# Optimization experiments

Measured on AMD Instinct MI355X. Metric: run time of the kernel, lower is better.

Reference implementation:

```python
import jax, jax.numpy as jnp
import numpy as np

# Physical parameter bounds in PARAM_NAMES order:
# [S1_max,S2_max,f_tens,f_rchr,f_base,r1,ku,c,alpha,psi,kappa,ki,ks,n,v,v_A,v_B,
#  Ac_max,b,lambda,chi,mu_t,T_rain,T_melt,melt_rate,lapse_rate,opg,MFMAX,MFMIN]
LOW = jnp.array([50.0,100.0,0.05,0.05,0.05,0.05,0.01,1.0,1.0,1.0,0.05,0.01,0.001,1.0,
                 0.001,0.001,0.001,0.05,0.001,5.0,2.0,0.01,-2.0,-2.0,1.0,-9.8,0.0,1.0,0.0],
                dtype=jnp.float32)
HIGH = jnp.array([5000.0,10000.0,0.95,0.95,0.95,0.95,1000.0,20.0,250.0,5.0,0.95,1000.0,
                  10000.0,10.0,0.25,0.25,0.25,0.95,3.0,10.0,5.0,5.0,4.0,4.0,10.0,0.0,1.0,10.0,10.0],
                 dtype=jnp.float32)
ROUTE_SHAPE = 2.5   # gamma routing shape (init kwarg)
KERNEL_LEN = 64     # routing kernel support (timesteps)
DT = 1.0
S1_INIT, S2_INIT = 50.0, 250.0  # state_init in the module


def _physical(raw_params):
    # low + (high-low)*sigmoid(raw), same as get_physical_params
    return LOW + (HIGH - LOW) * jax.nn.sigmoid(raw_params)


def _simulate(forcing, p):
    """Explicit-Euler 2-reservoir FUSE-style simulation. forcing: [T,3]=(prcp,pet,temp)."""
    S1_max, S2_max = p[0], p[1]
    f_tens, ku, c = p[2], p[6], p[7]
    ki, ks, n_exp = p[11], p[12], p[13]
    b, T_rain = p[18], p[22]

    def step(state, f):
        S1, S2 = state
        prcp, pet, temp = f[0], f[1], f[2]
        rain = jnp.where(temp > T_rain, prcp, 0.0)
        s1f = jnp.clip(S1 / S1_max, 0.0, 1.0)
        s2f = jnp.clip(S2 / S2_max, 0.0, 1.0)
        e1 = pet * jnp.minimum(s1f / f_tens, 1.0)          # tension-store evap
        qsx = rain * s1f ** b                               # saturation-excess runoff
        q12 = ku * s1f ** c                                 # percolation to lower store
        qif = ki * s1f                                      # interflow
        qb = ks * s2f ** n_exp                              # nonlinear baseflow
        S1n = jnp.clip(S1 + DT * (rain - qsx - e1 - q12 - qif), 0.0, S1_max)
        S2n = jnp.clip(S2 + DT * (q12 - qb), 0.0, S2_max)
        return (S1n, S2n), qsx + qif + qb

    init = (jnp.float32(S1_INIT), jnp.float32(S2_INIT))
    _, runoff = jax.lax.scan(step, init, forcing)
    return runoff  # [T]


def _route(runoff, shape, delay):
    """Causal gamma-kernel routing convolution (route_runoff)."""
    t = jnp.arange(KERNEL_LEN, dtype=jnp.float32) + 0.5
    theta = jnp.maximum(delay, 1e-3) / shape               # scale so mean = delay
    logk = (shape - 1.0) * jnp.log(t) - t / theta
    kern = jax.nn.softmax(logk)                            # normalized gamma weights
    return jnp.convolve(runoff, kern)[: runoff.shape[0]]   # causal conv


def reference(forcing, raw_params):
    phys = _physical(raw_params)
    runoff = _simulate(forcing, phys)
    # delay is used as a detached python float in the torch code -> stop_gradient
    delay = jax.lax.stop_gradient(phys[21])  # mu_t
    return _route(runoff, ROUTE_SHAPE, delay)


def setup_inputs() -> dict:
    key = jax.random.key(0)
    k1, k2, k3 = jax.random.split(key, 3)
    T = 131072
    prcp = jnp.maximum(jax.random.normal(k1, (T,)) * 5.0 + 2.0, 0.0)  # mm/day
    pet = jax.random.uniform(k2, (T,)) * 5.0                          # mm/day
    temp = jax.random.normal(k3, (T,)) * 8.0 + 5.0                    # deg C
    forcing = jnp.stack([prcp, pet, temp], axis=-1).astype(jnp.float32)
    raw_params = jnp.zeros((29,), dtype=jnp.float32)  # sigmoid(0)=0.5 -> mid-bounds
    return {"forcing": forcing, "raw_params": raw_params}
```

## Files before the change

### kernel.cpp

```cpp
#include <hip/hip_runtime.h>

#define KLEN 64
#define FCH 16
#define WARMUP 64
#define WIN_FC 64
#define S1_INIT_V 50.0f
#define S2_INIT_V 250.0f

__device__ __forceinline__ float fpow(float x, float e) {
    return exp2f(e * __log2f(x));
}
__device__ __forceinline__ float clamp01(float x) { return fminf(fmaxf(x, 0.0f), 1.0f); }
__device__ __forceinline__ float physp(const float* raw, int i, float lo, float hi) {
    return lo + (hi - lo) / (1.0f + __expf(-raw[i]));
}

struct F8 { float4 v[6]; };
__device__ __forceinline__ F8 load_f8(const float* __restrict__ forc, int t) {
    const float4* p = (const float4*)(forc + 3 * t);
    F8 r;
#pragma unroll
    for (int k = 0; k < 6; ++k) r.v[k] = p[k];
    return r;
}
__device__ __forceinline__ float f4c(const float4& v, int c) {
    return c == 0 ? v.x : c == 1 ? v.y : c == 2 ? v.z : v.w;
}
__device__ __forceinline__ float f8_get(const F8& f, int i) { return f4c(f.v[i >> 2], i & 3); }

#define S1_CORE(pr, pe, te, QACC)                                         \
    {                                                                     \
        float rain = (te) > Train ? (pr) : 0.0f;                          \
        float s1f = clamp01(S1 * invS1);                                  \
        float lg = __log2f(s1f);                                          \
        float e1 = (pe)*fminf(s1f * invft, 1.0f);                         \
        float qsx = rain * exp2f(b * lg);                                 \
        float q12 = ku * exp2f(cc * lg);                                  \
        float qif = ki * s1f;                                             \
        S1 = fminf(fmaxf(S1 + rain - qsx - e1 - q12 - qif, 0.0f), S1max); \
        QACC;                                                             \
    }

__global__ void __launch_bounds__(64) k_s1(
        const float* __restrict__ forc, const float* __restrict__ raw,
        float* __restrict__ s1s, float* __restrict__ q12f, float* __restrict__ Qw,
        int T, int nfine) {
    int lane = threadIdx.x;
    int j = blockIdx.x * WIN_FC + lane;
    bool active = j < nfine;

    const float S1max  = physp(raw, 0, 50.0f, 5000.0f);
    const float f_tens = physp(raw, 2, 0.05f, 0.95f);
    const float ku     = physp(raw, 6, 0.01f, 1000.0f);
    const float cc     = physp(raw, 7, 1.0f, 20.0f);
    const float ki     = physp(raw, 11, 0.01f, 1000.0f);
    const float b      = physp(raw, 18, 0.001f, 3.0f);
    const float Train  = physp(raw, 22, -2.0f, 4.0f);
    const float invS1 = 1.0f / S1max, invft = 1.0f / f_tens;

    float S1 = S1_INIT_V;
    float Q = 0.0f;
    if (active) {
        int t0 = j * FCH;
        int tend = min(t0 + FCH, T);
        int ts = max(t0 - WARMUP, 0);

        int ngw = (t0 - ts) >> 3;
        F8 cur = load_f8(forc, ts);
        for (int g = 0; g < ngw; ++g) {
            F8 nxt = load_f8(forc, ts + 8 * (g + 1));
#pragma unroll
            for (int s = 0; s < 8; ++s) {
                float pr = f8_get(cur, 3 * s), pe = f8_get(cur, 3 * s + 1), te = f8_get(cur, 3 * s + 2);
                S1_CORE(pr, pe, te, );
            }
            cur = nxt;
        }
        s1s[j] = S1;

        int ngm = (tend - t0) >> 3;
        for (int g = 0; g < ngm; ++g) {
            F8 nxt = load_f8(forc, t0 + 8 * min(g + 1, ngm - 1));
#pragma unroll
            for (int s = 0; s < 8; ++s) {
                float pr = f8_get(cur, 3 * s), pe = f8_get(cur, 3 * s + 1), te = f8_get(cur, 3 * s + 2);
                S1_CORE(pr, pe, te, Q += q12);
            }
            cur = nxt;
        }
        for (int t = t0 + 8 * ngm; t < tend; ++t) {
            float pr = forc[3 * t], pe = forc[3 * t + 1], te = forc[3 * t + 2];
            S1_CORE(pr, pe, te, Q += q12);
        }
        q12f[j] = Q;
    }
    float s = Q;
#pragma unroll
    for (int o = 32; o >= 1; o >>= 1) s += __shfl_xor(s, o, 64);
    if (lane == 0) Qw[blockIdx.x] = s;
}

__global__ void __launch_bounds__(64) k_s2win(
        const float* __restrict__ raw, const float* __restrict__ Qw,
        const float* __restrict__ q12f,
        float* __restrict__ S2win, float* __restrict__ qbwin,
        float* __restrict__ s2fine, int* __restrict__ flag,
        int T, int nfine) {
    int lane = threadIdx.x;
    const float S2max = physp(raw, 1, 100.0f, 10000.0f);
    const float ks    = physp(raw, 12, 0.001f, 10000.0f);
    const float nn    = physp(raw, 13, 1.0f, 10.0f);
    const float invS2 = 1.0f / S2max;

    int NW = (nfine + WIN_FC - 1) / WIN_FC;
    int WSTEPS = WIN_FC * FCH;

    int w0 = 2 * lane, w1 = 2 * lane + 1;
    float L0 = (w0 < NW) ? (float)min(WSTEPS, T - WSTEPS * w0) : 0.0f;
    float L1 = (w1 < NW) ? (float)min(WSTEPS, T - WSTEPS * w1) : 0.0f;
    float Q0 = (w0 < NW) ? Qw[w0] : 0.0f;
    float Q1 = (w1 < NW) ? Qw[w1] : 0.0f;

    float qb0 = ks * fpow(clamp01(S2_INIT_V * invS2), nn);
    float qb1 = qb0;
    float S20 = S2_INIT_V, S21 = S2_INIT_V;
    bool picard_ok = (NW <= 128);
    if (picard_ok) {
        for (int it = 0; it < 12; ++it) {
            float d0 = Q0 - L0 * qb0;
            float d1 = Q1 - L1 * qb1;
            float pair = d0 + d1;
            float sc = pair;
#pragma unroll
            for (int o = 1; o < 64; o <<= 1) {
                float v = __shfl_up(sc, o, 64);
                if (lane >= o) sc += v;
            }
            float excl = sc - pair;
            S20 = S2_INIT_V + excl;
            S21 = S20 + d0;
            qb0 = ks * fpow(clamp01(S20 * invS2), nn);
            qb1 = ks * fpow(clamp01(S21 * invS2), nn);
        }
        bool bad = false;
        if (w0 < NW) bad |= (S20 - L0 * qb0 < 0.5f) || (S20 + Q0 > S2max - 0.5f);
        if (w1 < NW) bad |= (S21 - L1 * qb1 < 0.5f) || (S21 + Q1 > S2max - 0.5f);
        picard_ok = (__ballot(bad) == 0ULL);
    }
    if (picard_ok) {
        if (w0 < NW) { S2win[w0] = S20; qbwin[w0] = qb0; }
        if (w1 < NW) { S2win[w1] = S21; qbwin[w1] = qb1; }
        if (lane == 0) *flag = 0;
    } else if (lane == 0) {
        *flag = 1;
        float S2 = S2_INIT_V;
        for (int w = 0; w < NW; ++w) {
            float s2f = clamp01(S2 * invS2);
            float qb = ks * fpow(s2f, nn);
            S2win[w] = S2; qbwin[w] = qb;
            int i0 = w * WIN_FC, i1 = min(i0 + WIN_FC, nfine);
            for (int i = i0; i < i1; ++i) {
                s2fine[i] = S2;
                float steps = (float)min(FCH, T - FCH * i);
                S2 = fminf(fmaxf(S2 + q12f[i] - steps * qb, 0.0f), S2max);
            }
        }
    }
}

__global__ void __launch_bounds__(64) k_sim(
        const float* __restrict__ forc, const float* __restrict__ raw,
        const float* __restrict__ s1s, const float* __restrict__ q12f,
        const float* __restrict__ S2win, const float* __restrict__ qbwin,
        const float* __restrict__ s2fine, const int* __restrict__ flag,
        float* __restrict__ runoff, int T, int nfine) {
    int lane = threadIdx.x;
    int j = blockIdx.x * WIN_FC + lane;
    bool active = j < nfine;

    const float S1max  = physp(raw, 0, 50.0f, 5000.0f);
    const float S2max  = physp(raw, 1, 100.0f, 10000.0f);
    const float f_tens = physp(raw, 2, 0.05f, 0.95f);
    const float ku     = physp(raw, 6, 0.01f, 1000.0f);
    const float ki     = physp(raw, 11, 0.01f, 1000.0f);
    const float ks     = physp(raw, 12, 0.001f, 10000.0f);
    const float nn     = physp(raw, 13, 1.0f, 10.0f);
    const float cc     = physp(raw, 7, 1.0f, 20.0f);
    const float b      = physp(raw, 18, 0.001f, 3.0f);
    const float Train  = physp(raw, 22, -2.0f, 4.0f);
    const float invS1 = 1.0f / S1max, invS2 = 1.0f / S2max, invft = 1.0f / f_tens;

    float q = active ? q12f[j] : 0.0f;
    float S2;
    if (*flag) {
        S2 = active ? s2fine[j] : 0.0f;
    } else {
        float sc = q;
#pragma unroll
        for (int o = 1; o < 64; o <<= 1) {
            float v = __shfl_up(sc, o, 64);
            if (lane >= o) sc += v;
        }
        float excl = sc - q;
        S2 = S2win[blockIdx.x] + excl - qbwin[blockIdx.x] * (float)(FCH * lane);
        S2 = fminf(fmaxf(S2, 0.0f), S2max);
    }
    if (!active) return;

    float S1 = s1s[j];
    int t0 = j * FCH;
    int tend = min(t0 + FCH, T);

#define SIM_CORE(pr, pe, te, EMIT)                                        \
    {                                                                     \
        float rain = (te) > Train ? (pr) : 0.0f;                          \
        float s1f = clamp01(S1 * invS1);                                  \
        float s2f = clamp01(S2 * invS2);                                  \
        float lg = __log2f(s1f);                                          \
        float e1 = (pe)*fminf(s1f * invft, 1.0f);                         \
        float qsx = rain * exp2f(b * lg);                                 \
        float q12 = ku * exp2f(cc * lg);                                  \
        float qif = ki * s1f;                                             \
        float qb = ks * fpow(s2f, nn);                                    \
        EMIT;                                                             \
        S1 = fminf(fmaxf(S1 + rain - qsx - e1 - q12 - qif, 0.0f), S1max); \
        S2 = fminf(fmaxf(S2 + q12 - qb, 0.0f), S2max);                    \
    }

    int ngm = (tend - t0) >> 3;
    if (ngm > 0) {
        F8 cur = load_f8(forc, t0);
        for (int g = 0; g < ngm; ++g) {
            F8 nxt = load_f8(forc, t0 + 8 * min(g + 1, ngm - 1));
            float ro[8];
#pragma unroll
            for (int s = 0; s < 8; ++s) {
                float pr = f8_get(cur, 3 * s), pe = f8_get(cur, 3 * s + 1), te = f8_get(cur, 3 * s + 2);
                SIM_CORE(pr, pe, te, ro[s] = qsx + qif + qb);
            }
            float4* rp = (float4*)(runoff + t0 + 8 * g);
            rp[0] = make_float4(ro[0], ro[1], ro[2], ro[3]);
            rp[1] = make_float4(ro[4], ro[5], ro[6], ro[7]);
            cur = nxt;
        }
    }
    for (int t = t0 + 8 * ngm; t < tend; ++t) {
        float pr = forc[3 * t], pe = forc[3 * t + 1], te = forc[3 * t + 2];
        SIM_CORE(pr, pe, te, runoff[t] = qsx + qif + qb);
    }
}

__global__ void k_route(const float* __restrict__ runoff, const float* __restrict__ raw,
                        float* __restrict__ out, int T) {
    __shared__ float ls[256 + KLEN - 1];
    __shared__ float ker[KLEN];
    int tid = threadIdx.x;
    int base = blockIdx.x * 256;
    if (tid < 64) {
        float delay = physp(raw, 21, 0.01f, 5.0f);
        float theta = fmaxf(delay, 1e-3f) * (1.0f / 2.5f);
        float tt = (float)tid + 0.5f;
        float logk = 1.5f * __logf(tt) - tt / theta;
        float m = logk;
#pragma unroll
        for (int o = 32; o >= 1; o >>= 1) m = fmaxf(m, __shfl_xor(m, o, 64));
        float e = __expf(logk - m);
        float s = e;
#pragma unroll
        for (int o = 32; o >= 1; o >>= 1) s += __shfl_xor(s, o, 64);
        ker[tid] = e / s;
    }
    for (int i = tid; i < 256 + KLEN - 1; i += 256) {
        int t = base - (KLEN - 1) + i;
        ls[i] = (t >= 0 && t < T) ? runoff[t] : 0.0f;
    }
    __syncthreads();
    float acc = 0.0f;
#pragma unroll
    for (int k = 0; k < KLEN; ++k) acc += ker[k] * ls[tid + (KLEN - 1) - k];
    int t = base + tid;
    if (t < T) out[t] = acc;
}

extern "C" void kernel_launch(void* const* d_in, const int* in_sizes, int n_in,
                              void* d_out, int out_size, void* d_ws, size_t ws_size,
                              hipStream_t stream) {
    const float* forcing = (const float*)d_in[0];
    const float* raw = (const float*)d_in[1];
    float* out = (float*)d_out;
    float* ws = (float*)d_ws;

    int T = in_sizes[0] / 3;
    int nfine = (T + FCH - 1) / FCH;
    int NW = (nfine + WIN_FC - 1) / WIN_FC;
    int P = ((nfine + 7) / 8) * 8;
    int PW = ((NW + 7) / 8) * 8;

    float* s1s = ws;
    float* q12f = s1s + P;
    float* Qw = q12f + P;
    float* S2win = Qw + PW;
    float* qbwin = S2win + PW;
    float* s2fine = qbwin + PW;
    int* flag = (int*)(s2fine + P);
    float* runoff = (float*)(flag + 8);

    k_s1<<<NW, 64, 0, stream>>>(forcing, raw, s1s, q12f, Qw, T, nfine);
    k_s2win<<<1, 64, 0, stream>>>(raw, Qw, q12f, S2win, qbwin, s2fine, flag, T, nfine);
    k_sim<<<NW, 64, 0, stream>>>(forcing, raw, s1s, q12f, S2win, qbwin, s2fine, flag,
                                 runoff, T, nfine);
    k_route<<<(T + 255) / 256, 256, 0, stream>>>(runoff, raw, out, T);
}
```

Before: 73.59 us.

## Fuse S1 scan, S2 window solve, simulation and routing into one cooperative kernel

Replaces the four launches (S1 chunk pass, single-block S2 Picard solve, full simulation, routing) with one cooperative kernel that uses grid.sync between phases. Each thread keeps per-step q12 and qsx+qif in registers from the S1 pass, so the second pass only recomputes the S2 recurrence instead of re-reading forcing and recomputing S1. Every block redundantly runs the small S2 window solve into shared memory, and routing runs as a grid-stride loop after a second grid sync. The cost is two grid-wide barriers, higher register pressure from the per-thread arrays, and a fallback path where each block runs a long serial loop.

```diff
diff --git a/kernel.cpp b/kernel.cpp
--- a/kernel.cpp
+++ b/kernel.cpp
@@ -1,9 +1,14 @@
 #include <hip/hip_runtime.h>
+#include <hip/hip_cooperative_groups.h>
+
+namespace cg = cooperative_groups;
 
 #define KLEN 64
 #define FCH 16
 #define WARMUP 64
 #define WIN_FC 64
+#define BLOCK 256
+#define WPB (BLOCK / 64)
 #define S1_INIT_V 50.0f
 #define S2_INIT_V 250.0f
 
@@ -41,31 +46,48 @@
         QACC;                                                             \
     }
 
-__global__ void __launch_bounds__(64) k_s1(
+__global__ void __launch_bounds__(BLOCK) k_fused(
         const float* __restrict__ forc, const float* __restrict__ raw,
-        float* __restrict__ s1s, float* __restrict__ q12f, float* __restrict__ Qw,
+        float* __restrict__ out,
+        float* __restrict__ q12f, float* __restrict__ Qw, float* __restrict__ runoff,
         int T, int nfine) {
-    int lane = threadIdx.x;
-    int j = blockIdx.x * WIN_FC + lane;
-    bool active = j < nfine;
+    cg::grid_group grid = cg::this_grid();
+
+    __shared__ float S2w_l[128], qbw_l[128];
+    __shared__ float s2f_l[BLOCK];
+    __shared__ float ker[KLEN];
+    __shared__ float ls[BLOCK + KLEN - 1];
+    __shared__ int flag_l;
+
+    const int tid = threadIdx.x;
+    const int lane = tid & 63;
+    const int wv = tid >> 6;
+    const int w = blockIdx.x * WPB + wv;
+    const int j = w * WIN_FC + lane;
+    const int NW = (nfine + WIN_FC - 1) / WIN_FC;
+    const bool active = j < nfine;
 
     const float S1max  = physp(raw, 0, 50.0f, 5000.0f);
+    const float S2max  = physp(raw, 1, 100.0f, 10000.0f);
     const float f_tens = physp(raw, 2, 0.05f, 0.95f);
     const float ku     = physp(raw, 6, 0.01f, 1000.0f);
     const float cc     = physp(raw, 7, 1.0f, 20.0f);
     const float ki     = physp(raw, 11, 0.01f, 1000.0f);
+    const float ks     = physp(raw, 12, 0.001f, 10000.0f);
+    const float nn     = physp(raw, 13, 1.0f, 10.0f);
     const float b      = physp(raw, 18, 0.001f, 3.0f);
     const float Train  = physp(raw, 22, -2.0f, 4.0f);
-    const float invS1 = 1.0f / S1max, invft = 1.0f / f_tens;
-
-    float S1 = S1_INIT_V;
+    const float invS1 = 1.0f / S1max, invS2 = 1.0f / S2max, invft = 1.0f / f_tens;
+
+    float q12s[FCH], qxi[FCH];
     float Q = 0.0f;
     if (active) {
-        int t0 = j * FCH;
-        int tend = min(t0 + FCH, T);
+        const int t0 = j * FCH;
+        const bool full = (t0 + FCH <= T);
+        float S1 = S1_INIT_V;
         int ts = max(t0 - WARMUP, 0);
-
         int ngw = (t0 - ts) >> 3;
+
         F8 cur = load_f8(forc, ts);
         for (int g = 0; g < ngw; ++g) {
             F8 nxt = load_f8(forc, ts + 8 * (g + 1));
@@ -76,186 +98,143 @@
             }
             cur = nxt;
         }
-        s1s[j] = S1;
-
-        int ngm = (tend - t0) >> 3;
-        for (int g = 0; g < ngm; ++g) {
-            F8 nxt = load_f8(forc, t0 + 8 * min(g + 1, ngm - 1));
-#pragma unroll
-            for (int s = 0; s < 8; ++s) {
-                float pr = f8_get(cur, 3 * s), pe = f8_get(cur, 3 * s + 1), te = f8_get(cur, 3 * s + 2);
-                S1_CORE(pr, pe, te, Q += q12);
-            }
-            cur = nxt;
-        }
-        for (int t = t0 + 8 * ngm; t < tend; ++t) {
-            float pr = forc[3 * t], pe = forc[3 * t + 1], te = forc[3 * t + 2];
-            S1_CORE(pr, pe, te, Q += q12);
+        if (full) {
+#pragma unroll
+            for (int g = 0; g < FCH / 8; ++g) {
+                F8 nxt = cur;
+                if (g + 1 < FCH / 8) nxt = load_f8(forc, t0 + 8 * (g + 1));
+#pragma unroll
+                for (int s = 0; s < 8; ++s) {
+                    float pr = f8_get(cur, 3 * s), pe = f8_get(cur, 3 * s + 1), te = f8_get(cur, 3 * s + 2);
+                    S1_CORE(pr, pe, te, q12s[8 * g + s] = q12; qxi[8 * g + s] = qsx + qif; Q += q12);
+                }
+                cur = nxt;
+            }
+        } else {
+#pragma unroll
+            for (int s = 0; s < FCH; ++s) {
+                int t = t0 + s;
+                if (t < T) {
+                    float pr = forc[3 * t], pe = forc[3 * t + 1], te = forc[3 * t + 2];
+                    S1_CORE(pr, pe, te, q12s[s] = q12; qxi[s] = qsx + qif; Q += q12);
+                } else {
+                    q12s[s] = 0.0f; qxi[s] = 0.0f;
+                }
+            }
         }
         q12f[j] = Q;
     }
-    float s = Q;
-#pragma unroll
-    for (int o = 32; o >= 1; o >>= 1) s += __shfl_xor(s, o, 64);
-    if (lane == 0) Qw[blockIdx.x] = s;
-}
-
-__global__ void __launch_bounds__(64) k_s2win(
-        const float* __restrict__ raw, const float* __restrict__ Qw,
-        const float* __restrict__ q12f,
-        float* __restrict__ S2win, float* __restrict__ qbwin,
-        float* __restrict__ s2fine, int* __restrict__ flag,
-        int T, int nfine) {
-    int lane = threadIdx.x;
-    const float S2max = physp(raw, 1, 100.0f, 10000.0f);
-    const float ks    = physp(raw, 12, 0.001f, 10000.0f);
-    const float nn    = physp(raw, 13, 1.0f, 10.0f);
-    const float invS2 = 1.0f / S2max;
-
-    int NW = (nfine + WIN_FC - 1) / WIN_FC;
-    int WSTEPS = WIN_FC * FCH;
-
-    int w0 = 2 * lane, w1 = 2 * lane + 1;
-    float L0 = (w0 < NW) ? (float)min(WSTEPS, T - WSTEPS * w0) : 0.0f;
-    float L1 = (w1 < NW) ? (float)min(WSTEPS, T - WSTEPS * w1) : 0.0f;
-    float Q0 = (w0 < NW) ? Qw[w0] : 0.0f;
-    float Q1 = (w1 < NW) ? Qw[w1] : 0.0f;
-
-    float qb0 = ks * fpow(clamp01(S2_INIT_V * invS2), nn);
-    float qb1 = qb0;
-    float S20 = S2_INIT_V, S21 = S2_INIT_V;
-    bool picard_ok = (NW <= 128);
-    if (picard_ok) {
-        for (int it = 0; it < 12; ++it) {
-            float d0 = Q0 - L0 * qb0;
-            float d1 = Q1 - L1 * qb1;
-            float pair = d0 + d1;
-            float sc = pair;
-#pragma unroll
-            for (int o = 1; o < 64; o <<= 1) {
-                float v = __shfl_up(sc, o, 64);
-                if (lane >= o) sc += v;
-            }
-            float excl = sc - pair;
-            S20 = S2_INIT_V + excl;
-            S21 = S20 + d0;
-            qb0 = ks * fpow(clamp01(S20 * invS2), nn);
-            qb1 = ks * fpow(clamp01(S21 * invS2), nn);
-        }
-        bool bad = false;
-        if (w0 < NW) bad |= (S20 - L0 * qb0 < 0.5f) || (S20 + Q0 > S2max - 0.5f);
-        if (w1 < NW) bad |= (S21 - L1 * qb1 < 0.5f) || (S21 + Q1 > S2max - 0.5f);
-        picard_ok = (__ballot(bad) == 0ULL);
-    }
-    if (picard_ok) {
-        if (w0 < NW) { S2win[w0] = S20; qbwin[w0] = qb0; }
-        if (w1 < NW) { S2win[w1] = S21; qbwin[w1] = qb1; }
-        if (lane == 0) *flag = 0;
-    } else if (lane == 0) {
-        *flag = 1;
-        float S2 = S2_INIT_V;
-        for (int w = 0; w < NW; ++w) {
-            float s2f = clamp01(S2 * invS2);
-            float qb = ks * fpow(s2f, nn);
-            S2win[w] = S2; qbwin[w] = qb;
-            int i0 = w * WIN_FC, i1 = min(i0 + WIN_FC, nfine);
-            for (int i = i0; i < i1; ++i) {
-                s2fine[i] = S2;
-                float steps = (float)min(FCH, T - FCH * i);
-                S2 = fminf(fmaxf(S2 + q12f[i] - steps * qb, 0.0f), S2max);
-            }
-        }
-    }
-}
-
-__global__ void __launch_bounds__(64) k_sim(
-        const float* __restrict__ forc, const float* __restrict__ raw,
-        const float* __restrict__ s1s, const float* __restrict__ q12f,
-        const float* __restrict__ S2win, const float* __restrict__ qbwin,
-        const float* __restrict__ s2fine, const int* __restrict__ flag,
-        float* __restrict__ runoff, int T, int nfine) {
-    int lane = threadIdx.x;
-    int j = blockIdx.x * WIN_FC + lane;
-    bool active = j < nfine;
-
-    const float S1max  = physp(raw, 0, 50.0f, 5000.0f);
-    const float S2max  = physp(raw, 1, 100.0f, 10000.0f);
-    const float f_tens = physp(raw, 2, 0.05f, 0.95f);
-    const float ku     = physp(raw, 6, 0.01f, 1000.0f);
-    const float ki     = physp(raw, 11, 0.01f, 1000.0f);
-    const float ks     = physp(raw, 12, 0.001f, 10000.0f);
-    const float nn     = physp(raw, 13, 1.0f, 10.0f);
-    const float cc     = physp(raw, 7, 1.0f, 20.0f);
-    const float b      = physp(raw, 18, 0.001f, 3.0f);
-    const float Train  = physp(raw, 22, -2.0f, 4.0f);
-    const float invS1 = 1.0f / S1max, invS2 = 1.0f / S2max, invft = 1.0f / f_tens;
-
-    float q = active ? q12f[j] : 0.0f;
-    float S2;
-    if (*flag) {
-        S2 = active ? s2fine[j] : 0.0f;
-    } else {
-        float sc = q;
+    {
+        float sq = Q;
+#pragma unroll
+        for (int o = 32; o >= 1; o >>= 1) sq += __shfl_xor(sq, o, 64);
+        if (lane == 0 && w < NW) Qw[w] = sq;
+    }
+
+    grid.sync();
+
+    if (wv == 0) {
+        const int WSTEPS = WIN_FC * FCH;
+        int w0 = 2 * lane, w1 = 2 * lane + 1;
+        float L0 = (w0 < NW) ? (float)min(WSTEPS, T - WSTEPS * w0) : 0.0f;
+        float L1 = (w1 < NW) ? (float)min(WSTEPS, T - WSTEPS * w1) : 0.0f;
+        float Q0 = (w0 < NW) ? Qw[w0] : 0.0f;
+        float Q1 = (w1 < NW) ? Qw[w1] : 0.0f;
+
+        float qb0 = ks * fpow(clamp01(S2_INIT_V * invS2), nn);
+        float qb1 = qb0;
+        float S20 = S2_INIT_V, S21 = S2_INIT_V;
+        bool picard_ok = (NW <= 128);
+        if (picard_ok) {
+            for (int it = 0; it < 12; ++it) {
+                float d0 = Q0 - L0 * qb0;
+                float d1 = Q1 - L1 * qb1;
+                float pair = d0 + d1;
+                float sc = pair;
+#pragma unroll
+                for (int o = 1; o < 64; o <<= 1) {
+                    float v = __shfl_up(sc, o, 64);
+                    if (lane >= o) sc += v;
+                }
+                float excl = sc - pair;
+                S20 = S2_INIT_V + excl;
+                S21 = S20 + d0;
+                qb0 = ks * fpow(clamp01(S20 * invS2), nn);
+                qb1 = ks * fpow(clamp01(S21 * invS2), nn);
+            }
+            bool bad = false;
+            if (w0 < NW) bad |= (S20 - L0 * qb0 < 0.5f) || (S20 + Q0 > S2max - 0.5f);
+            if (w1 < NW) bad |= (S21 - L1 * qb1 < 0.5f) || (S21 + Q1 > S2max - 0.5f);
+            picard_ok = (__ballot(bad) == 0ULL);
+        }
+        if (picard_ok) {
+            if (w0 < NW) { S2w_l[w0] = S20; qbw_l[w0] = qb0; }
+            if (w1 < NW) { S2w_l[w1] = S21; qbw_l[w1] = qb1; }
+            if (lane == 0) flag_l = 0;
+        } else if (lane == 0) {
+            flag_l = 1;
+            float S2 = S2_INIT_V;
+            int blk0 = blockIdx.x * BLOCK;
+            for (int ww = 0; ww < NW; ++ww) {
+                float s2fw = clamp01(S2 * invS2);
+                float qb = ks * fpow(s2fw, nn);
+                int i0 = ww * WIN_FC, i1 = min(i0 + WIN_FC, nfine);
+                for (int i = i0; i < i1; ++i) {
+                    if ((unsigned)(i - blk0) < (unsigned)BLOCK) s2f_l[i - blk0] = S2;
+                    float steps = (float)min(FCH, T - FCH * i);
+                    S2 = fminf(fmaxf(S2 + q12f[i] - steps * qb, 0.0f), S2max);
+                }
+            }
+        }
+    }
+    __syncthreads();
+
+    {
+        float sc = Q;
 #pragma unroll
         for (int o = 1; o < 64; o <<= 1) {
             float v = __shfl_up(sc, o, 64);
             if (lane >= o) sc += v;
         }
-        float excl = sc - q;
-        S2 = S2win[blockIdx.x] + excl - qbwin[blockIdx.x] * (float)(FCH * lane);
-        S2 = fminf(fmaxf(S2, 0.0f), S2max);
-    }
-    if (!active) return;
-
-    float S1 = s1s[j];
-    int t0 = j * FCH;
-    int tend = min(t0 + FCH, T);
-
-#define SIM_CORE(pr, pe, te, EMIT)                                        \
-    {                                                                     \
-        float rain = (te) > Train ? (pr) : 0.0f;                          \
-        float s1f = clamp01(S1 * invS1);                                  \
-        float s2f = clamp01(S2 * invS2);                                  \
-        float lg = __log2f(s1f);                                          \
-        float e1 = (pe)*fminf(s1f * invft, 1.0f);                         \
-        float qsx = rain * exp2f(b * lg);                                 \
-        float q12 = ku * exp2f(cc * lg);                                  \
-        float qif = ki * s1f;                                             \
-        float qb = ks * fpow(s2f, nn);                                    \
-        EMIT;                                                             \
-        S1 = fminf(fmaxf(S1 + rain - qsx - e1 - q12 - qif, 0.0f), S1max); \
-        S2 = fminf(fmaxf(S2 + q12 - qb, 0.0f), S2max);                    \
-    }
-
-    int ngm = (tend - t0) >> 3;
-    if (ngm > 0) {
-        F8 cur = load_f8(forc, t0);
-        for (int g = 0; g < ngm; ++g) {
-            F8 nxt = load_f8(forc, t0 + 8 * min(g + 1, ngm - 1));
-            float ro[8];
-#pragma unroll
-            for (int s = 0; s < 8; ++s) {
-                float pr = f8_get(cur, 3 * s), pe = f8_get(cur, 3 * s + 1), te = f8_get(cur, 3 * s + 2);
-                SIM_CORE(pr, pe, te, ro[s] = qsx + qif + qb);
-            }
-            float4* rp = (float4*)(runoff + t0 + 8 * g);
-            rp[0] = make_float4(ro[0], ro[1], ro[2], ro[3]);
-            rp[1] = make_float4(ro[4], ro[5], ro[6], ro[7]);
-            cur = nxt;
-        }
-    }
-    for (int t = t0 + 8 * ngm; t < tend; ++t) {
-        float pr = forc[3 * t], pe = forc[3 * t + 1], te = forc[3 * t + 2];
-        SIM_CORE(pr, pe, te, runoff[t] = qsx + qif + qb);
-    }
-}
-
-__global__ void k_route(const float* __restrict__ runoff, const float* __restrict__ raw,
-                        float* __restrict__ out, int T) {
-    __shared__ float ls[256 + KLEN - 1];
-    __shared__ float ker[KLEN];
-    int tid = threadIdx.x;
-    int base = blockIdx.x * 256;
+        float excl = sc - Q;
+        if (active) {
+            float S2;
+            if (flag_l) {
+                S2 = s2f_l[tid];
+            } else {
+                S2 = S2w_l[w] + excl - qbw_l[w] * (float)(FCH * lane);
+                S2 = fminf(fmaxf(S2, 0.0f), S2max);
+            }
+            int t0 = j * FCH;
+            bool full = (t0 + FCH <= T);
+            if (full) {
+                float ro[FCH];
+#pragma unroll
+                for (int s = 0; s < FCH; ++s) {
+                    float s2f = clamp01(S2 * invS2);
+                    float qb = ks * fpow(s2f, nn);
+                    ro[s] = qxi[s] + qb;
+                    S2 = fminf(fmaxf(S2 + q12s[s] - qb, 0.0f), S2max);
+                }
+                float4* rp = (float4*)(runoff + t0);
+#pragma unroll
+                for (int v4 = 0; v4 < FCH / 4; ++v4)
+                    rp[v4] = make_float4(ro[4 * v4], ro[4 * v4 + 1], ro[4 * v4 + 2], ro[4 * v4 + 3]);
+            } else {
+#pragma unroll
+                for (int s = 0; s < FCH; ++s) {
+                    int t = t0 + s;
+                    if (t < T) {
+                        float s2f = clamp01(S2 * invS2);
+                        float qb = ks * fpow(s2f, nn);
+                        runoff[t] = qxi[s] + qb;
+                        S2 = fminf(fmaxf(S2 + q12s[s] - qb, 0.0f), S2max);
+                    }
+                }
+            }
+        }
+    }
+
     if (tid < 64) {
         float delay = physp(raw, 21, 0.01f, 5.0f);
         float theta = fmaxf(delay, 1e-3f) * (1.0f / 2.5f);
@@ -270,16 +249,24 @@
         for (int o = 32; o >= 1; o >>= 1) s += __shfl_xor(s, o, 64);
         ker[tid] = e / s;
     }
-    for (int i = tid; i < 256 + KLEN - 1; i += 256) {
-        int t = base - (KLEN - 1) + i;
-        ls[i] = (t >= 0 && t < T) ? runoff[t] : 0.0f;
-    }
-    __syncthreads();
-    float acc = 0.0f;
-#pragma unroll
-    for (int k = 0; k < KLEN; ++k) acc += ker[k] * ls[tid + (KLEN - 1) - k];
-    int t = base + tid;
-    if (t < T) out[t] = acc;
+
+    grid.sync();
+
+    int ntile = (T + BLOCK - 1) / BLOCK;
+    for (int tile = blockIdx.x; tile < ntile; tile += gridDim.x) {
+        int base = tile * BLOCK;
+        __syncthreads();
+        for (int i = tid; i < BLOCK + KLEN - 1; i += BLOCK) {
+            int t = base - (KLEN - 1) + i;
+            ls[i] = (t >= 0 && t < T) ? runoff[t] : 0.0f;
+        }
+        __syncthreads();
+        float acc = 0.0f;
+#pragma unroll
+        for (int k = 0; k < KLEN; ++k) acc += ker[k] * ls[tid + (KLEN - 1) - k];
+        int t = base + tid;
+        if (t < T) out[t] = acc;
+    }
 }
 
 extern "C" void kernel_launch(void* const* d_in, const int* in_sizes, int n_in,
@@ -293,21 +280,18 @@
     int T = in_sizes[0] / 3;
     int nfine = (T + FCH - 1) / FCH;
     int NW = (nfine + WIN_FC - 1) / WIN_FC;
+    int nblocks = (NW + WPB - 1) / WPB;
+    if (nblocks < 1) nblocks = 1;
+
     int P = ((nfine + 7) / 8) * 8;
     int PW = ((NW + 7) / 8) * 8;
-
-    float* s1s = ws;
-    float* q12f = s1s + P;
+    float* q12f = ws;
     float* Qw = q12f + P;
-    float* S2win = Qw + PW;
-    float* qbwin = S2win + PW;
-    float* s2fine = qbwin + PW;
-    int* flag = (int*)(s2fine + P);
-    float* runoff = (float*)(flag + 8);
-
-    k_s1<<<NW, 64, 0, stream>>>(forcing, raw, s1s, q12f, Qw, T, nfine);
-    k_s2win<<<1, 64, 0, stream>>>(raw, Qw, q12f, S2win, qbwin, s2fine, flag, T, nfine);
-    k_sim<<<NW, 64, 0, stream>>>(forcing, raw, s1s, q12f, S2win, qbwin, s2fine, flag,
-                                 runoff, T, nfine);
-    k_route<<<(T + 255) / 256, 256, 0, stream>>>(runoff, raw, out, T);
-}
+    float* runoff = Qw + PW;
+
+    void* args[] = { (void*)&forcing, (void*)&raw, (void*)&out,
+                     (void*)&q12f, (void*)&Qw, (void*)&runoff,
+                     (void*)&T, (void*)&nfine };
+    hipLaunchCooperativeKernel((const void*)k_fused, dim3(nblocks), dim3(BLOCK),
+                               args, 0, stream);
+}
```

Result: slower. 114.8 us (+56.1%).
